# Performance work log

Measured on AMD Instinct MI355X. Metric: run time of the kernel, lower is better.

Reference implementation:

```python
import jax, jax.numpy as jnp
import numpy as np
from jax import lax

B_BLK = 16   # block size B
N_Z = 64     # latent dim


def setup_inputs() -> dict:
    key = jax.random.key(0)
    ks = jax.random.split(key, 6)
    in_ch, out_ch = 256, 256
    L = (out_ch // B_BLK) * (in_ch // B_BLK)  # 256 latent codes
    x = jax.random.normal(ks[0], (32, in_ch, 64, 64), dtype=jnp.float32)
    z = jax.random.normal(ks[1], (L, N_Z), dtype=jnp.float32)
    W1 = jax.random.normal(ks[2], (B_BLK, N_Z, N_Z), dtype=jnp.float32) * 0.1
    B1 = jax.random.normal(ks[3], (B_BLK, N_Z), dtype=jnp.float32) * 0.1
    W2 = jax.random.normal(ks[4], (B_BLK, B_BLK * 9, N_Z), dtype=jnp.float32) * 0.1
    B2 = jax.random.normal(ks[5], (B_BLK, B_BLK * 9), dtype=jnp.float32) * 0.1
    return {"x": x, "z": z, "W1": W1, "B1": B1, "W2": W2, "B2": B2}


def _aggregate_weight(z, W1, B1, W2, B2, out_ch, in_ch):
    # hypertype='separate', batched over all L = (out_ch//B)*(in_ch//B) blocks.
    # per block: a = W1 @ z + B1 -> (B, N_z); K = W2 @ a[...,None] + B2 -> (B, B*9)
    a = jnp.einsum('bdn,ln->lbd', W1, z) + B1            # (L, B, N_z)
    K = jnp.einsum('bkd,lbd->lbk', W2, a) + B2           # (L, B, B*9)
    ob, ib = out_ch // B_BLK, in_ch // B_BLK
    K = K.reshape(ob, ib, B_BLK, B_BLK, 3, 3)            # (o_blk, i_blk, b1, b2, 3, 3)
    # torch: K.reshape(B,B,3,3).permute(1,0,2,3) => weight_block[p,q] = K[q,p]
    # then cat over i_blk on dim 1 (in), over o_blk on dim 0 (out)
    w = K.transpose(0, 3, 1, 2, 4, 5)                    # (o_blk, b2, i_blk, b1, 3, 3)
    return w.reshape(out_ch, in_ch, 3, 3)


def reference(x, z, W1, B1, W2, B2):
    out_ch, in_ch = 256, 256
    weight = _aggregate_weight(z, W1, B1, W2, B2, out_ch, in_ch)
    # F.conv2d(x, weight, bias=None, stride=1, padding=kernel_size//2=1)
    return lax.conv_general_dilated(
        x, weight,
        window_strides=(1, 1),
        padding=[(1, 1), (1, 1)],
        dimension_numbers=('NCHW', 'OIHW', 'NCHW'))
```

## Files before the change

kernel.cpp:

```cpp
#include <hip/hip_runtime.h>

typedef unsigned short u16;
typedef unsigned int u32;
typedef __attribute__((ext_vector_type(8))) short short8;
typedef __attribute__((ext_vector_type(4))) float f32x4;

__device__ __forceinline__ u16 f2bf(float f) {
    u32 u = __float_as_uint(f);
    return (u16)((u + 0x7FFFu + ((u >> 16) & 1u)) >> 16);
}

#define COMP(f4, e) ((e) == 0 ? (f4).x : (e) == 1 ? (f4).y : (e) == 2 ? (f4).z : (f4).w)

__device__ __forceinline__ void gld16(const u16* g, u16* l) {
    __builtin_amdgcn_global_load_lds(
        (const __attribute__((address_space(1))) unsigned int*)(unsigned long long)(const void*)g,
        (__attribute__((address_space(3))) unsigned int*)(unsigned long long)(void*)l,
        16, 0, 0);
}

__global__ __launch_bounds__(256) void nchw2nhwc_pad(const float* __restrict__ x,
                                                     u16* __restrict__ xp) {
    __shared__ __align__(16) u16 T[64][264];
    const int tid = threadIdx.x;
    const int b   = blockIdx.x;
    const int n   = b >> 6;
    const int row = b & 63;
    const int g16 = tid >> 4;
    const int pxq = tid & 15;

    const float* src = x + ((size_t)n * 256 + g16 * 16) * 4096 + row * 64 + pxq * 4;
    float4 v[4][4];
#pragma unroll
    for (int u = 0; u < 4; ++u)
#pragma unroll
        for (int i = 0; i < 4; ++i)
            v[u][i] = *(const float4*)(src + (size_t)(u * 4 + i) * 4096);

#pragma unroll
    for (int u = 0; u < 4; ++u) {
        const int ic = g16 * 16 + u * 4;
#pragma unroll
        for (int e = 0; e < 4; ++e) {
            const int px = pxq * 4 + e;
            const u32 lo = ((u32)f2bf(COMP(v[u][1], e)) << 16) | f2bf(COMP(v[u][0], e));
            const u32 hi = ((u32)f2bf(COMP(v[u][3], e)) << 16) | f2bf(COMP(v[u][2], e));
            *(uint2*)&T[px][ic] = make_uint2(lo, hi);
        }
    }
    __syncthreads();

    const int c = tid & 31, p0 = tid >> 5;
    u16* dstN = xp + ((size_t)n * 4356 + (size_t)(row + 1) * 66 + 1) * 256 + c * 8;
#pragma unroll
    for (int pp = 0; pp < 8; ++pp) {
        const int px = pp * 8 + p0;
        *(uint4*)(dstN + (size_t)px * 256) = *(const uint4*)&T[px][c * 8];
    }

    u16* hrow = xp + ((size_t)n * 4356 + (size_t)(row + 1) * 66) * 256;
    if (tid < 64) {
        const int wp = (tid >> 5) ? 65 : 0;
        uint4 zz = {0u, 0u, 0u, 0u};
        *(uint4*)(hrow + (size_t)wp * 256 + (tid & 31) * 8) = zz;
    }
    if (row == 0) {
        u16* tb = xp + (size_t)n * 4356 * 256;
        uint4 zz = {0u, 0u, 0u, 0u};
        for (int i = tid; i < 2112; i += 256) *(uint4*)(tb + (size_t)i * 8) = zz;
    }
    if (row == 63) {
        u16* bb = xp + ((size_t)n * 4356 + 65 * 66) * 256;
        uint4 zz = {0u, 0u, 0u, 0u};
        for (int i = tid; i < 2112; i += 256) *(uint4*)(bb + (size_t)i * 8) = zz;
    }
}

__global__ __launch_bounds__(256) void wgen(const float* __restrict__ z,
                                            const float* __restrict__ W1,
                                            const float* __restrict__ B1,
                                            const float* __restrict__ W2,
                                            const float* __restrict__ B2,
                                            u16* __restrict__ wb) {
    __shared__ float zl[64][65];
    __shared__ float w1s[4096];
    __shared__ float aS[64][65];
    __shared__ float w2s[9216];

    const int tid = threadIdx.x;
    const int b   = blockIdx.x >> 2;
    const int lc  = blockIdx.x & 3;
    const int l   = tid & 63;
    const int g   = tid >> 6;

    const float* zg  = z  + (size_t)lc * 4096;
    const float* w1g = W1 + (size_t)b * 4096;
    const float* w2g = W2 + (size_t)b * 9216;
#pragma unroll
    for (int k = 0; k < 4; ++k) {
        const int i4 = tid + k * 256;
        const float4 v = *(const float4*)(zg + (size_t)i4 * 4);
        const int lr = i4 >> 4, nr = (i4 * 4) & 63;
        zl[lr][nr] = v.x; zl[lr][nr + 1] = v.y; zl[lr][nr + 2] = v.z; zl[lr][nr + 3] = v.w;
        *(float4*)(w1s + (size_t)i4 * 4) = *(const float4*)(w1g + (size_t)i4 * 4);
    }
#pragma unroll
    for (int k = 0; k < 9; ++k) {
        const int i4 = tid + k * 256;
        *(float4*)(w2s + (size_t)i4 * 4) = *(const float4*)(w2g + (size_t)i4 * 4);
    }
    __syncthreads();

    {
        float acc[16];
#pragma unroll
        for (int j = 0; j < 16; ++j) acc[j] = B1[b * 64 + g * 16 + j];
#pragma unroll
        for (int nb = 0; nb < 16; ++nb) {
            float zv0 = zl[l][nb * 4 + 0];
            float zv1 = zl[l][nb * 4 + 1];
            float zv2 = zl[l][nb * 4 + 2];
            float zv3 = zl[l][nb * 4 + 3];
#pragma unroll
            for (int j = 0; j < 16; ++j) {
                const float4 w = *(const float4*)(w1s + (g * 16 + j) * 64 + nb * 4);
                acc[j] += w.x * zv0 + w.y * zv1 + w.z * zv2 + w.w * zv3;
            }
        }
#pragma unroll
        for (int j = 0; j < 16; ++j) aS[l][g * 16 + j] = acc[j];
    }
    __syncthreads();

    float acc2[36];
#pragma unroll
    for (int t = 0; t < 36; ++t) acc2[t] = B2[b * 144 + g * 36 + t];
#pragma unroll
    for (int db = 0; db < 16; ++db) {
        float av0 = aS[l][db * 4 + 0];
        float av1 = aS[l][db * 4 + 1];
        float av2 = aS[l][db * 4 + 2];
        float av3 = aS[l][db * 4 + 3];
#pragma unroll
        for (int t = 0; t < 36; ++t) {
            const float4 w = *(const float4*)(w2s + (g * 36 + t) * 64 + db * 4);
            acc2[t] += w.x * av0 + w.y * av1 + w.z * av2 + w.w * av3;
        }
    }

    const int lg = lc * 64 + l;
    const int ob = lg >> 4, ib = lg & 15;
#pragma unroll
    for (int t = 0; t < 36; ++t) {
        const int b2 = 4 * g + t / 9;
        const int tap = t % 9;
        wb[(size_t)(ob * 16 + b2) * 2304 + tap * 256 + ib * 16 + b] = f2bf(acc2[t]);
    }
}

__global__ __launch_bounds__(512, 2) void conv_mfma(const u16* __restrict__ xp,
                                                    const u16* __restrict__ wb,
                                                    float* __restrict__ out) {
    __shared__ __align__(16) u16 As[4][8192];
    __shared__ __align__(16) u16 Bs[4][8192];

    const int tid  = threadIdx.x;
    const int b0   = blockIdx.x;
    const int bid  = (b0 & 7) * 64 + (b0 >> 3);
    const int n    = bid >> 4;
    const int pimg = (bid & 15) << 8;
    const int lane = tid & 63;
    const int wave = tid >> 6;
    const int wm = wave >> 2;
    const int wn = wave & 3;
    const int lr = lane & 15, lq = lane >> 4;

    const int prw = tid >> 3;
    const int psl = tid & 7;
    const int sl  = psl ^ (prw & 7);
    const int s4o = (sl & 3) * 8;
    const int par = sl >> 2;
    const int ocA0 = (prw)      * 2 + par;
    const int ocA1 = (64 + prw) * 2 + par;
    const u16* aG0 = wb + (size_t)ocA0 * 2304 + s4o;
    const u16* aG1 = wb + (size_t)ocA1 * 2304 + s4o;
    const int pxB0 = (prw)      * 2 + par;
    const int pxB1 = (64 + prw) * 2 + par;
    const int prow0 = (bid & 15) * 4;
    const int pb0 = (prow0 + (pxB0 >> 6) + 1) * 66 + (pxB0 & 63) + 1;
    const int pb1 = (prow0 + (pxB1 >> 6) + 1) * 66 + (pxB1 & 63) + 1;
    const u16* xpN = xp + (size_t)n * 4356 * 256 + s4o;
    const int ldst = wave * 512;

    f32x4 acc[8][4];
    const f32x4 z4 = {0.f, 0.f, 0.f, 0.f};
#pragma unroll
    for (int i = 0; i < 8; ++i)
#pragma unroll
        for (int j = 0; j < 4; ++j) acc[i][j] = z4;

    auto stage = [&](int t) {
        const int s = t & 3;
        const int tap = t >> 3, icb = t & 7;
        const int t3 = tap / 3;
        const int dh = t3 - 1, dw = tap - t3 * 3 - 1;
        const int ko = tap * 256 + icb * 32;
        const int bo = (dh * 66 + dw) * 256 + icb * 32;
        u16* as_ = &As[s][ldst];
        u16* bs_ = &Bs[s][ldst];
        gld16(aG0 + ko, as_);
        gld16(aG1 + ko, as_ + 4096);
        gld16(xpN + (pb0 * 256 + bo), bs_);
        gld16(xpN + (pb1 * 256 + bo), bs_ + 4096);
    };

    auto compute = [&](int t) {
        const int s = t & 3;
        const u16* Ab = &As[s][0];
        const u16* Bb = &Bs[s][0];
        short8 bfr[4];
#pragma unroll
        for (int j = 0; j < 4; ++j) {
            const int px = wn * 64 + j * 16 + lr;
            const int pr = px >> 1;
            const int ps = (((px & 1) << 2) | lq) ^ (pr & 7);
            bfr[j] = *(const short8*)(Bb + pr * 64 + ps * 8);
        }
#pragma unroll
        for (int mh = 0; mh < 2; ++mh) {
            short8 afr[4];
#pragma unroll
            for (int i = 0; i < 4; ++i) {
                const int oc = wm * 128 + mh * 64 + i * 16 + lr;
                const int pr = oc >> 1;
                const int ps = (((oc & 1) << 2) | lq) ^ (pr & 7);
                afr[i] = *(const short8*)(Ab + pr * 64 + ps * 8);
            }
            __builtin_amdgcn_s_setprio(1);
#pragma unroll
            for (int i = 0; i < 4; ++i)
#pragma unroll
                for (int j = 0; j < 4; ++j)
                    acc[mh * 4 + i][j] = __builtin_amdgcn_mfma_f32_16x16x32_bf16(
                        afr[i], bfr[j], acc[mh * 4 + i][j], 0, 0, 0);
            __builtin_amdgcn_s_setprio(0);
        }
    };

    stage(0); stage(1); stage(2);

#pragma unroll 1
    for (int t = 0; t < 69; ++t) {
        asm volatile("s_waitcnt vmcnt(8)" ::: "memory");
        __builtin_amdgcn_s_barrier();
        asm volatile("" ::: "memory");
        compute(t);
        stage(t + 3);
    }
    asm volatile("s_waitcnt vmcnt(8)" ::: "memory");
    __builtin_amdgcn_s_barrier();
    asm volatile("" ::: "memory");
    compute(69);
    asm volatile("s_waitcnt vmcnt(4)" ::: "memory");
    __builtin_amdgcn_s_barrier();
    asm volatile("" ::: "memory");
    compute(70);
    asm volatile("s_waitcnt vmcnt(0)" ::: "memory");
    __builtin_amdgcn_s_barrier();
    asm volatile("" ::: "memory");
    compute(71);

    const size_t outn = (size_t)n * 256 * 4096;
#pragma unroll
    for (int mi = 0; mi < 8; ++mi) {
        const int ocb = wm * 128 + mi * 16 + lq * 4;
#pragma unroll
        for (int j = 0; j < 4; ++j) {
            const int po = pimg + wn * 64 + j * 16 + lr;
            float* op = out + outn + (size_t)ocb * 4096 + po;
#pragma unroll
            for (int r = 0; r < 4; ++r) op[(size_t)r * 4096] = acc[mi][j][r];
        }
    }
}

extern "C" void kernel_launch(void* const* d_in, const int* in_sizes, int n_in,
                              void* d_out, int out_size, void* d_ws, size_t ws_size,
                              hipStream_t stream) {
    const float* x  = (const float*)d_in[0];
    const float* z  = (const float*)d_in[1];
    const float* W1 = (const float*)d_in[2];
    const float* B1 = (const float*)d_in[3];
    const float* W2 = (const float*)d_in[4];
    const float* B2 = (const float*)d_in[5];
    float* out = (float*)d_out;

    u16* xp = (u16*)d_ws;
    u16* wb = xp + (size_t)32 * 4356 * 256;
    const size_t need = ((size_t)32 * 4356 * 256 + (size_t)256 * 2304) * 2;
    if (ws_size < need) return;

    nchw2nhwc_pad<<<dim3(2048), dim3(256), 0, stream>>>(x, xp);
    wgen<<<dim3(64), dim3(256), 0, stream>>>(z, W1, B1, W2, B2, wb);
    conv_mfma<<<dim3(512), dim3(512), 0, stream>>>(xp, wb, out);
}
```

Before: 392.7 us.

## Interleave split global-to-LDS loads with MFMA halves in the conv main loop

Restructures the main GEMM loop so that each iteration issues the A-tile prefetch after the first half of LDS fragment reads and the B-tile prefetch after the second half. Extra barriers separate the halves, and the wait/barrier for the next stage moves to the end of the iteration. The goal is to spread global_load_lds traffic across the MFMA work and shorten the exposed wait at each stage boundary. The cost is three barriers per iteration instead of one, and correctness now relies on the 4-stage ring keeping the stage being overwritten distinct from the stage being read.

```diff
diff --git a/kernel.cpp b/kernel.cpp
--- a/kernel.cpp
+++ b/kernel.cpp
@@ -199,7 +199,7 @@
 #pragma unroll
         for (int j = 0; j < 4; ++j) acc[i][j] = z4;
 
-    auto stage = [&](int t) {
+    auto stage_full = [&](int t) {
         const int s = t & 3;
         const int tap = t >> 3, icb = t & 7;
         const int t3 = tap / 3;
@@ -214,11 +214,24 @@
         gld16(xpN + (pb1 * 256 + bo), bs_ + 4096);
     };
 
-    auto compute = [&](int t) {
+    stage_full(0); stage_full(1); stage_full(2);
+    asm volatile("s_waitcnt vmcnt(8)" ::: "memory");
+    __builtin_amdgcn_s_barrier();
+    asm volatile("" ::: "memory");
+
+#pragma unroll 1
+    for (int t = 0; t < 72; ++t) {
+        const int tf = t + 3;
+        const int tapf = tf >> 3, icbf = tf & 7;
+        const int t3f = tapf / 3;
+        const int kof = tapf * 256 + icbf * 32;
+        const int bof = ((t3f - 1) * 66 + (tapf - t3f * 3 - 1)) * 256 + icbf * 32;
+        const int sf = tf & 3;
         const int s = t & 3;
         const u16* Ab = &As[s][0];
         const u16* Bb = &Bs[s][0];
-        short8 bfr[4];
+
+        short8 bfr[4], afr[4];
 #pragma unroll
         for (int j = 0; j < 4; ++j) {
             const int px = wn * 64 + j * 16 + lr;
@@ -227,48 +240,59 @@
             bfr[j] = *(const short8*)(Bb + pr * 64 + ps * 8);
         }
 #pragma unroll
-        for (int mh = 0; mh < 2; ++mh) {
-            short8 afr[4];
-#pragma unroll
-            for (int i = 0; i < 4; ++i) {
-                const int oc = wm * 128 + mh * 64 + i * 16 + lr;
-                const int pr = oc >> 1;
-                const int ps = (((oc & 1) << 2) | lq) ^ (pr & 7);
-                afr[i] = *(const short8*)(Ab + pr * 64 + ps * 8);
-            }
-            __builtin_amdgcn_s_setprio(1);
-#pragma unroll
-            for (int i = 0; i < 4; ++i)
-#pragma unroll
-                for (int j = 0; j < 4; ++j)
-                    acc[mh * 4 + i][j] = __builtin_amdgcn_mfma_f32_16x16x32_bf16(
-                        afr[i], bfr[j], acc[mh * 4 + i][j], 0, 0, 0);
-            __builtin_amdgcn_s_setprio(0);
-        }
-    };
-
-    stage(0); stage(1); stage(2);
-
-#pragma unroll 1
-    for (int t = 0; t < 69; ++t) {
-        asm volatile("s_waitcnt vmcnt(8)" ::: "memory");
+        for (int i = 0; i < 4; ++i) {
+            const int oc = wm * 128 + i * 16 + lr;
+            const int pr = oc >> 1;
+            const int ps = (((oc & 1) << 2) | lq) ^ (pr & 7);
+            afr[i] = *(const short8*)(Ab + pr * 64 + ps * 8);
+        }
+        if (t < 69) {
+            u16* as_ = &As[sf][ldst];
+            gld16(aG0 + kof, as_);
+            gld16(aG1 + kof, as_ + 4096);
+        }
+        asm volatile("" ::: "memory");
         __builtin_amdgcn_s_barrier();
         asm volatile("" ::: "memory");
-        compute(t);
-        stage(t + 3);
-    }
-    asm volatile("s_waitcnt vmcnt(8)" ::: "memory");
-    __builtin_amdgcn_s_barrier();
-    asm volatile("" ::: "memory");
-    compute(69);
-    asm volatile("s_waitcnt vmcnt(4)" ::: "memory");
-    __builtin_amdgcn_s_barrier();
-    asm volatile("" ::: "memory");
-    compute(70);
-    asm volatile("s_waitcnt vmcnt(0)" ::: "memory");
-    __builtin_amdgcn_s_barrier();
-    asm volatile("" ::: "memory");
-    compute(71);
+        __builtin_amdgcn_s_setprio(1);
+#pragma unroll
+        for (int i = 0; i < 4; ++i)
+#pragma unroll
+            for (int j = 0; j < 4; ++j)
+                acc[i][j] = __builtin_amdgcn_mfma_f32_16x16x32_bf16(
+                    afr[i], bfr[j], acc[i][j], 0, 0, 0);
+        __builtin_amdgcn_s_setprio(0);
+
+#pragma unroll
+        for (int i = 0; i < 4; ++i) {
+            const int oc = wm * 128 + 64 + i * 16 + lr;
+            const int pr = oc >> 1;
+            const int ps = (((oc & 1) << 2) | lq) ^ (pr & 7);
+            afr[i] = *(const short8*)(Ab + pr * 64 + ps * 8);
+        }
+        if (t < 69) {
+            u16* bs_ = &Bs[sf][ldst];
+            gld16(xpN + (pb0 * 256 + bof), bs_);
+            gld16(xpN + (pb1 * 256 + bof), bs_ + 4096);
+        }
+        asm volatile("" ::: "memory");
+        __builtin_amdgcn_s_barrier();
+        asm volatile("" ::: "memory");
+        __builtin_amdgcn_s_setprio(1);
+#pragma unroll
+        for (int i = 0; i < 4; ++i)
+#pragma unroll
+            for (int j = 0; j < 4; ++j)
+                acc[4 + i][j] = __builtin_amdgcn_mfma_f32_16x16x32_bf16(
+                    afr[i], bfr[j], acc[4 + i][j], 0, 0, 0);
+        __builtin_amdgcn_s_setprio(0);
+
+        if (t < 69)       asm volatile("s_waitcnt vmcnt(8)" ::: "memory");
+        else if (t == 69) asm volatile("s_waitcnt vmcnt(4)" ::: "memory");
+        else if (t == 70) asm volatile("s_waitcnt vmcnt(0)" ::: "memory");
+        __builtin_amdgcn_s_barrier();
+        asm volatile("" ::: "memory");
+    }
 
     const size_t outn = (size_t)n * 256 * 4096;
 #pragma unroll
```

Result: slower. 404.5 us (+3.0%).

## Switch conv GEMM to 32x32x16 MFMA with 4 waves per 256x256 tile

Applied to the files above, without the earlier changes.

Rewrites the implicit-GEMM conv kernel to use 32x32x16 bf16 MFMA instructions. The block shrinks from 8 to 4 waves, each owning a 128x128 output sub-tile. This is meant to raise MFMA efficiency and cut LDS fragment reads per FLOP, and the staging and epilogue are rewritten to match. In exchange each wave holds 256 accumulator registers and occupancy drops to one 256-thread block per CU, which may expose load latency.

```diff
diff --git a/kernel.cpp b/kernel.cpp
--- a/kernel.cpp
+++ b/kernel.cpp
@@ -3,7 +3,7 @@
 typedef unsigned short u16;
 typedef unsigned int u32;
 typedef __attribute__((ext_vector_type(8))) short short8;
-typedef __attribute__((ext_vector_type(4))) float f32x4;
+typedef __attribute__((ext_vector_type(16))) float f32x16;
 
 __device__ __forceinline__ u16 f2bf(float f) {
     u32 u = __float_as_uint(f);
@@ -158,7 +158,7 @@
     }
 }
 
-__global__ __launch_bounds__(512, 2) void conv_mfma(const u16* __restrict__ xp,
+__global__ __launch_bounds__(256, 1) void conv_mfma(const u16* __restrict__ xp,
                                                     const u16* __restrict__ wb,
                                                     float* __restrict__ out) {
     __shared__ __align__(16) u16 As[4][8192];
@@ -171,78 +171,76 @@
     const int pimg = (bid & 15) << 8;
     const int lane = tid & 63;
     const int wave = tid >> 6;
-    const int wm = wave >> 2;
-    const int wn = wave & 3;
-    const int lr = lane & 15, lq = lane >> 4;
-
-    const int prw = tid >> 3;
-    const int psl = tid & 7;
-    const int sl  = psl ^ (prw & 7);
-    const int s4o = (sl & 3) * 8;
-    const int par = sl >> 2;
-    const int ocA0 = (prw)      * 2 + par;
-    const int ocA1 = (64 + prw) * 2 + par;
-    const u16* aG0 = wb + (size_t)ocA0 * 2304 + s4o;
-    const u16* aG1 = wb + (size_t)ocA1 * 2304 + s4o;
-    const int pxB0 = (prw)      * 2 + par;
-    const int pxB1 = (64 + prw) * 2 + par;
-    const int prow0 = (bid & 15) * 4;
-    const int pb0 = (prow0 + (pxB0 >> 6) + 1) * 66 + (pxB0 & 63) + 1;
-    const int pb1 = (prow0 + (pxB1 >> 6) + 1) * 66 + (pxB1 & 63) + 1;
-    const u16* xpN = xp + (size_t)n * 4356 * 256 + s4o;
-    const int ldst = wave * 512;
-
-    f32x4 acc[8][4];
-    const f32x4 z4 = {0.f, 0.f, 0.f, 0.f};
-#pragma unroll
-    for (int i = 0; i < 8; ++i)
-#pragma unroll
-        for (int j = 0; j < 4; ++j) acc[i][j] = z4;
+    const int wm2  = wave >> 1;
+    const int wn2  = wave & 1;
+    const int l31  = lane & 31, l5 = lane >> 5;
+
+    const int swb    = (lane & 7) ^ (lane >> 3);
+    const int par    = swb >> 2;
+    const int kc     = swb & 3;
+    const int rowoff = 2 * (lane >> 3) + par;
+    const u16* aBase = wb + (size_t)(wave * 16 + rowoff) * 2304 + kc * 8;
+    const int prow_img0 = (bid & 15) * 4;
+    int pbq[4];
+#pragma unroll
+    for (int q = 0; q < 4; ++q)
+        pbq[q] = (prow_img0 + 1 + q) * 66 + wave * 16 + rowoff + 1;
+    const u16* xpN = xp + (size_t)n * 4356 * 256 + kc * 8;
+    const int ldw = wave * 512;
+
+    const int prA  = wm2 * 64 + (l31 >> 1);
+    const int prB  = wn2 * 64 + (l31 >> 1);
+    const int psx  = (((l31 & 1) << 2)) ^ 0;
+    const int pr7  = (l31 >> 1) & 7;
+    const int psk0 = (((l31 & 1) << 2) | (0 + l5)) ^ pr7;
+    const int psk1 = (((l31 & 1) << 2) | (2 + l5)) ^ pr7;
+    (void)psx;
+
+    f32x16 acc[4][4];
+#pragma unroll
+    for (int i = 0; i < 4; ++i)
+#pragma unroll
+        for (int j = 0; j < 4; ++j)
+#pragma unroll
+            for (int r = 0; r < 16; ++r) acc[i][j][r] = 0.f;
 
     auto stage = [&](int t) {
         const int s = t & 3;
         const int tap = t >> 3, icb = t & 7;
         const int t3 = tap / 3;
-        const int dh = t3 - 1, dw = tap - t3 * 3 - 1;
         const int ko = tap * 256 + icb * 32;
-        const int bo = (dh * 66 + dw) * 256 + icb * 32;
-        u16* as_ = &As[s][ldst];
-        u16* bs_ = &Bs[s][ldst];
-        gld16(aG0 + ko, as_);
-        gld16(aG1 + ko, as_ + 4096);
-        gld16(xpN + (pb0 * 256 + bo), bs_);
-        gld16(xpN + (pb1 * 256 + bo), bs_ + 4096);
+        const int bo = ((t3 - 1) * 66 + (tap - t3 * 3 - 1)) * 256 + icb * 32;
+        const u16* aS_ = aBase + ko;
+#pragma unroll
+        for (int q = 0; q < 4; ++q)
+            gld16(aS_ + (size_t)q * 64 * 2304, &As[s][q * 2048 + ldw]);
+        const u16* bS_ = xpN + bo;
+#pragma unroll
+        for (int q = 0; q < 4; ++q)
+            gld16(bS_ + (size_t)pbq[q] * 256, &Bs[s][q * 2048 + ldw]);
     };
 
     auto compute = [&](int t) {
         const int s = t & 3;
         const u16* Ab = &As[s][0];
         const u16* Bb = &Bs[s][0];
-        short8 bfr[4];
-#pragma unroll
-        for (int j = 0; j < 4; ++j) {
-            const int px = wn * 64 + j * 16 + lr;
-            const int pr = px >> 1;
-            const int ps = (((px & 1) << 2) | lq) ^ (pr & 7);
-            bfr[j] = *(const short8*)(Bb + pr * 64 + ps * 8);
-        }
-#pragma unroll
-        for (int mh = 0; mh < 2; ++mh) {
-            short8 afr[4];
-#pragma unroll
-            for (int i = 0; i < 4; ++i) {
-                const int oc = wm * 128 + mh * 64 + i * 16 + lr;
-                const int pr = oc >> 1;
-                const int ps = (((oc & 1) << 2) | lq) ^ (pr & 7);
-                afr[i] = *(const short8*)(Ab + pr * 64 + ps * 8);
-            }
+#pragma unroll
+        for (int ks = 0; ks < 2; ++ks) {
+            const int ps = ks ? psk1 : psk0;
+            short8 afr[4], bfr[4];
+#pragma unroll
+            for (int i = 0; i < 4; ++i)
+                afr[i] = *(const short8*)(Ab + (prA + i * 16) * 64 + ps * 8);
+#pragma unroll
+            for (int j = 0; j < 4; ++j)
+                bfr[j] = *(const short8*)(Bb + (prB + j * 16) * 64 + ps * 8);
             __builtin_amdgcn_s_setprio(1);
 #pragma unroll
             for (int i = 0; i < 4; ++i)
 #pragma unroll
                 for (int j = 0; j < 4; ++j)
-                    acc[mh * 4 + i][j] = __builtin_amdgcn_mfma_f32_16x16x32_bf16(
-                        afr[i], bfr[j], acc[mh * 4 + i][j], 0, 0, 0);
+                    acc[i][j] = __builtin_amdgcn_mfma_f32_32x32x16_bf16(
+                        afr[i], bfr[j], acc[i][j], 0, 0, 0);
             __builtin_amdgcn_s_setprio(0);
         }
     };
@@ -250,36 +248,29 @@
     stage(0); stage(1); stage(2);
 
 #pragma unroll 1
-    for (int t = 0; t < 69; ++t) {
-        asm volatile("s_waitcnt vmcnt(8)" ::: "memory");
+    for (int t = 0; t < 72; ++t) {
+        if (t < 70)       asm volatile("s_waitcnt vmcnt(16)" ::: "memory");
+        else if (t == 70) asm volatile("s_waitcnt vmcnt(8)" ::: "memory");
+        else              asm volatile("s_waitcnt vmcnt(0)" ::: "memory");
         __builtin_amdgcn_s_barrier();
         asm volatile("" ::: "memory");
         compute(t);
-        stage(t + 3);
-    }
-    asm volatile("s_waitcnt vmcnt(8)" ::: "memory");
-    __builtin_amdgcn_s_barrier();
-    asm volatile("" ::: "memory");
-    compute(69);
-    asm volatile("s_waitcnt vmcnt(4)" ::: "memory");
-    __builtin_amdgcn_s_barrier();
-    asm volatile("" ::: "memory");
-    compute(70);
-    asm volatile("s_waitcnt vmcnt(0)" ::: "memory");
-    __builtin_amdgcn_s_barrier();
-    asm volatile("" ::: "memory");
-    compute(71);
+        if (t < 69) stage(t + 3);
+    }
 
     const size_t outn = (size_t)n * 256 * 4096;
-#pragma unroll
-    for (int mi = 0; mi < 8; ++mi) {
-        const int ocb = wm * 128 + mi * 16 + lq * 4;
+    const int px0  = pimg + wn2 * 128 + l31;
+    const int oc00 = wm2 * 128 + 4 * l5;
+#pragma unroll
+    for (int i = 0; i < 4; ++i) {
 #pragma unroll
         for (int j = 0; j < 4; ++j) {
-            const int po = pimg + wn * 64 + j * 16 + lr;
-            float* op = out + outn + (size_t)ocb * 4096 + po;
-#pragma unroll
-            for (int r = 0; r < 4; ++r) op[(size_t)r * 4096] = acc[mi][j][r];
+            float* op = out + outn + px0 + j * 32;
+#pragma unroll
+            for (int rg = 0; rg < 16; ++rg) {
+                const int oc = oc00 + i * 32 + (rg & 3) + 8 * (rg >> 2);
+                op[(size_t)oc * 4096] = acc[i][j][rg];
+            }
         }
     }
 }
@@ -302,5 +293,5 @@
 
     nchw2nhwc_pad<<<dim3(2048), dim3(256), 0, stream>>>(x, xp);
     wgen<<<dim3(64), dim3(256), 0, stream>>>(z, W1, B1, W2, B2, wb);
-    conv_mfma<<<dim3(512), dim3(512), 0, stream>>>(xp, wb, out);
-}
+    conv_mfma<<<dim3(512), dim3(256), 0, stream>>>(xp, wb, out);
+}
```

New measurement: 477.7 us. +21.6%, slower.
